# Kernel tuning notes

Hardware: AMD Instinct MI355X
Metric: run time of the kernel (lower is better)

The kernel has to match this reference:

```python
import jax, jax.numpy as jnp
import numpy as np


def _params_to_tokens(params):
    # (batch, 2k) -> (batch, k, 2) : chunk into freqs/amps then stack
    freqs, amps = jnp.split(params, 2, axis=-1)
    return jnp.stack((freqs, amps), axis=-1)


def setup_inputs() -> dict:
    key = jax.random.key(0)
    k1, k2 = jax.random.split(key)
    predicted = jax.random.normal(k1, (64, 4096), dtype=jnp.float32)
    target = jax.random.normal(k2, (64, 4096), dtype=jnp.float32)
    return {"predicted": predicted, "target": target}


def reference(predicted, target):
    p = _params_to_tokens(predicted)   # (b, k, 2)
    t = _params_to_tokens(target)      # (b, k, 2)
    # Euclidean cdist via gram-matrix identity (avoids (b,k,k,2) broadcast temp)
    p2 = jnp.sum(p * p, axis=-1)       # (b, k)
    t2 = jnp.sum(t * t, axis=-1)       # (b, k)
    gram = jnp.einsum('bid,bjd->bij', p, t)  # (b, k, k)
    sq = p2[:, :, None] + t2[:, None, :] - 2.0 * gram
    costs = jnp.sqrt(jnp.maximum(sq, 0.0))   # (b, k, k)
    min1 = jnp.mean(jnp.min(costs, axis=1), axis=-1)  # min over predicted dim
    min2 = jnp.mean(jnp.min(costs, axis=2), axis=-1)  # min over target dim
    return jnp.mean(min1 + min2)
```

## Files before the change

kernel.cpp:

```cpp
#include <hip/hip_runtime.h>


typedef _Float16 f16;
typedef _Float16 f16x8 __attribute__((ext_vector_type(8)));
typedef float f32x16 __attribute__((ext_vector_type(16)));

constexpr int K = 2048;
constexpr int BLOCK = 512;
constexpr int NBAND = 8;
constexpr int BAND = 256;
constexpr int NJT = K / 32;
constexpr unsigned INF_U = 0x7F800000u;

#define MFMA16 __builtin_amdgcn_mfma_f32_32x32x16_f16

__device__ __forceinline__ unsigned pk(f16 lo, f16 hi) {
  unsigned a = (unsigned)__builtin_bit_cast(unsigned short, lo);
  unsigned b = (unsigned)__builtin_bit_cast(unsigned short, hi);
  return a | (b << 16);
}
__device__ __forceinline__ unsigned split2(float v) {
  const f16 h = (f16)v;
  const f16 l = (f16)(v - (float)h);
  return pk(h, l);
}
__device__ __forceinline__ unsigned duplo(unsigned u) { return (u & 0xffffu) | (u << 16); }
__device__ __forceinline__ unsigned duphi(unsigned u) { return (u >> 16) | (u & 0xffff0000u); }
__device__ __forceinline__ f16x8 bcast4(unsigned d) {
  uint4 t = make_uint4(d, d, d, d);
  return __builtin_bit_cast(f16x8, t);
}
__device__ __forceinline__ float min3p(float a, float b, float c) {
  return fminf(fminf(a, b), c);
}

__global__ __launch_bounds__(BLOCK, 4) void chamfer_mfma(
    const float* __restrict__ pred, const float* __restrict__ targ,
    float* __restrict__ out, float* __restrict__ ws) {
  const int iband = blockIdx.x;
  const int b = blockIdx.y;
  const int tid = threadIdx.x;
  const int lane = tid & 63;
  const int w = tid >> 6;
  const int r = lane & 31;

  __shared__ uint4 Brec[K];
  __shared__ uint4 Arec[BAND];
  __shared__ unsigned colmin_u[K];
  __shared__ float wsum[8];

  const float* tb = targ + (size_t)b * (2 * K);
  const float* pb = pred + (size_t)b * (2 * K);

  #pragma unroll
  for (int k = 0; k < K / BLOCK; ++k) {
    const int j = tid + k * BLOCK;
    const float x = tb[j], y = tb[K + j];
    Brec[j] = make_uint4(split2(x), split2(y), split2(fmaf(x, x, y * y)), 0u);
    colmin_u[j] = INF_U;
  }
  if (tid < BAND) {
    const int i = iband * BAND + tid;
    const float x = pb[i], y = pb[K + i];
    Arec[tid] = make_uint4(split2(-2.0f * x), split2(-2.0f * y),
                           split2(fmaf(x, x, y * y)), 0u);
  }
  __syncthreads();

  const f32x16 zero = {};
  const unsigned umask = (lane < 32) ? 0xFFFFFFFFu : 0u;
  const unsigned umask_lo = umask & 0xFFFFu;

  const uint4 ra = Arec[w * 32 + r];
  const f16x8 aUH = bcast4(duplo(ra.x)), aUL = bcast4(duphi(ra.x));
  const f16x8 aWH = bcast4(duplo(ra.y)), aWL = bcast4(duphi(ra.y));
  const f16x8 aONE = bcast4(0x3C003C00u);

  uint4 bs = make_uint4(0x3C00u & umask, 0u, 0u, 0u);
  f32x16 seed = MFMA16(bcast4(duplo(ra.z)), __builtin_bit_cast(f16x8, bs),
                       zero, 0, 0, 0);
  seed = MFMA16(bcast4(duphi(ra.z)), __builtin_bit_cast(f16x8, bs),
                seed, 0, 0, 0);

  f32x16 rowacc;
  #pragma unroll
  for (int q = 0; q < 16; ++q) rowacc[q] = 3.4e38f;

  uint4 bq0 = make_uint4(0u, 0u, 0u, 0u);
  uint4 bq1 = make_uint4(0u, 0u, 0u, 0u);

  for (int jt = 0; jt < NJT; jt += 2) {
    const uint4 rb0 = Brec[jt * 32 + r];
    const uint4 rb1 = Brec[jt * 32 + 32 + r];

    bq0.x = rb0.x & umask;
    f32x16 d0 = MFMA16(aUH, __builtin_bit_cast(f16x8, bq0), seed, 0, 0, 0);
    bq0.x = rb0.x & umask_lo;
    d0 = MFMA16(aUL, __builtin_bit_cast(f16x8, bq0), d0, 0, 0, 0);
    bq0.x = rb0.y & umask;
    d0 = MFMA16(aWH, __builtin_bit_cast(f16x8, bq0), d0, 0, 0, 0);
    bq0.x = rb0.y & umask_lo;
    d0 = MFMA16(aWL, __builtin_bit_cast(f16x8, bq0), d0, 0, 0, 0);
    bq0.x = rb0.z & umask;
    d0 = MFMA16(aONE, __builtin_bit_cast(f16x8, bq0), d0, 0, 0, 0);

    bq1.x = rb1.x & umask;
    f32x16 d1 = MFMA16(aUH, __builtin_bit_cast(f16x8, bq1), seed, 0, 0, 0);
    bq1.x = rb1.x & umask_lo;
    d1 = MFMA16(aUL, __builtin_bit_cast(f16x8, bq1), d1, 0, 0, 0);
    bq1.x = rb1.y & umask;
    d1 = MFMA16(aWH, __builtin_bit_cast(f16x8, bq1), d1, 0, 0, 0);
    bq1.x = rb1.y & umask_lo;
    d1 = MFMA16(aWL, __builtin_bit_cast(f16x8, bq1), d1, 0, 0, 0);
    bq1.x = rb1.z & umask;
    d1 = MFMA16(aONE, __builtin_bit_cast(f16x8, bq1), d1, 0, 0, 0);

    #pragma unroll
    for (int q = 0; q < 16; ++q)
      rowacc[q] = min3p(rowacc[q], d0[q], d1[q]);

    {
      const float a0 = min3p(d0[0], d0[1], d0[2]);
      const float a1 = min3p(d0[3], d0[4], d0[5]);
      const float a2 = min3p(d0[6], d0[7], d0[8]);
      const float a3 = min3p(d0[9], d0[10], d0[11]);
      const float a4 = min3p(d0[12], d0[13], d0[14]);
      float cm = fminf(min3p(a0, a1, a2), min3p(a3, a4, d0[15]));
      cm = fminf(cm, __shfl_xor(cm, 32, 64));
      cm = fmaxf(cm, 0.0f);
      if (lane < 32) atomicMin(&colmin_u[jt * 32 + r], __float_as_uint(cm));
    }
    {
      const float a0 = min3p(d1[0], d1[1], d1[2]);
      const float a1 = min3p(d1[3], d1[4], d1[5]);
      const float a2 = min3p(d1[6], d1[7], d1[8]);
      const float a3 = min3p(d1[9], d1[10], d1[11]);
      const float a4 = min3p(d1[12], d1[13], d1[14]);
      float cm = fminf(min3p(a0, a1, a2), min3p(a3, a4, d1[15]));
      cm = fminf(cm, __shfl_xor(cm, 32, 64));
      cm = fmaxf(cm, 0.0f);
      if (lane < 32) atomicMin(&colmin_u[jt * 32 + 32 + r], __float_as_uint(cm));
    }
  }

  #pragma unroll
  for (int m = 1; m <= 16; m <<= 1) {
    #pragma unroll
    for (int q = 0; q < 16; ++q)
      rowacc[q] = fminf(rowacc[q], __shfl_xor(rowacc[q], m, 64));
  }
  float s = 0.0f;
  #pragma unroll
  for (int q = 0; q < 16; ++q) s += sqrtf(fmaxf(rowacc[q], 0.0f));
  s += __shfl_xor(s, 32, 64);
  if (lane == 0) wsum[w] = s;
  __syncthreads();
  if (tid == 0) {
    float t = 0.0f;
    #pragma unroll
    for (int i = 0; i < 8; ++i) t += wsum[i];
    atomicAdd(out, t * (1.0f / 131072.0f));
  }
  float* wrow = ws + (size_t)(b * NBAND + iband) * K;
  #pragma unroll
  for (int k = 0; k < K / BLOCK; ++k) {
    const int j = tid + k * BLOCK;
    wrow[j] = __uint_as_float(colmin_u[j]);
  }
}

__global__ __launch_bounds__(256, 4) void chamfer_pass2(
    const float* __restrict__ ws, float* __restrict__ out) {
  const int b = blockIdx.x;
  const int tid = threadIdx.x;
  __shared__ float wsum[4];
  const float* wrow = ws + (size_t)b * NBAND * K;
  float s = 0.0f;
  #pragma unroll
  for (int k = 0; k < K / 256; ++k) {
    const int j = tid + k * 256;
    float m = wrow[j];
    #pragma unroll
    for (int band = 1; band < NBAND; ++band) m = fminf(m, wrow[band * K + j]);
    s += sqrtf(m);
  }
  #pragma unroll
  for (int off = 32; off; off >>= 1) s += __shfl_down(s, off, 64);
  const int lane = tid & 63, w = tid >> 6;
  if (lane == 0) wsum[w] = s;
  __syncthreads();
  if (tid == 0)
    atomicAdd(out, (wsum[0] + wsum[1] + wsum[2] + wsum[3]) * (1.0f / 131072.0f));
}

extern "C" void kernel_launch(void* const* d_in, const int* in_sizes, int n_in,
                              void* d_out, int out_size, void* d_ws, size_t ws_size,
                              hipStream_t stream) {
  const float* pred = (const float*)d_in[0];
  const float* targ = (const float*)d_in[1];
  float* out = (float*)d_out;
  float* ws = (float*)d_ws;

  dim3 g1(NBAND, 64);
  chamfer_mfma<<<g1, dim3(BLOCK), 0, stream>>>(pred, targ, out, ws);
  chamfer_pass2<<<dim3(64), dim3(256), 0, stream>>>(ws, out);
}
```

Before: 93.80 us.

## Pack all distance terms into one MFMA K-dimension per tile

Replaces the five chained MFMAs per 32x32 tile (one per split term) and the seed MFMAs with a single 32x32x16 MFMA. The hi/lo fp16 split products, the squared norms and the ones column are packed across the 16-element K dimension using both lane halves. This cuts matrix-instruction count and the accumulator dependency chain about fivefold. The cost is extra per-iteration integer packing and lane selects, and the change relies on the packed operand layout exactly matching the MFMA K-index mapping.

```diff
diff --git a/kernel.cpp b/kernel.cpp
--- a/kernel.cpp
+++ b/kernel.cpp
@@ -24,12 +24,6 @@
   const f16 l = (f16)(v - (float)h);
   return pk(h, l);
 }
-__device__ __forceinline__ unsigned duplo(unsigned u) { return (u & 0xffffu) | (u << 16); }
-__device__ __forceinline__ unsigned duphi(unsigned u) { return (u >> 16) | (u & 0xffff0000u); }
-__device__ __forceinline__ f16x8 bcast4(unsigned d) {
-  uint4 t = make_uint4(d, d, d, d);
-  return __builtin_bit_cast(f16x8, t);
-}
 __device__ __forceinline__ float min3p(float a, float b, float c) {
   return fminf(fminf(a, b), c);
 }
@@ -43,6 +37,7 @@
   const int lane = tid & 63;
   const int w = tid >> 6;
   const int r = lane & 31;
+  const bool lo_half = (lane < 32);
 
   __shared__ uint4 Brec[K];
   __shared__ uint4 Arec[BAND];
@@ -68,52 +63,37 @@
   __syncthreads();
 
   const f32x16 zero = {};
-  const unsigned umask = (lane < 32) ? 0xFFFFFFFFu : 0u;
-  const unsigned umask_lo = umask & 0xFFFFu;
 
   const uint4 ra = Arec[w * 32 + r];
-  const f16x8 aUH = bcast4(duplo(ra.x)), aUL = bcast4(duphi(ra.x));
-  const f16x8 aWH = bcast4(duplo(ra.y)), aWL = bcast4(duphi(ra.y));
-  const f16x8 aONE = bcast4(0x3C003C00u);
-
-  uint4 bs = make_uint4(0x3C00u & umask, 0u, 0u, 0u);
-  f32x16 seed = MFMA16(bcast4(duplo(ra.z)), __builtin_bit_cast(f16x8, bs),
-                       zero, 0, 0, 0);
-  seed = MFMA16(bcast4(duphi(ra.z)), __builtin_bit_cast(f16x8, bs),
-                seed, 0, 0, 0);
+  const uint4 alo = make_uint4((ra.x & 0xffffu) | (ra.x << 16),
+                               (ra.x >> 16) | (ra.y << 16),
+                               ra.y,
+                               0x3C003C00u);
+  const uint4 ahi = make_uint4(ra.z, 0u, 0u, 0u);
+  const f16x8 af = __builtin_bit_cast(f16x8, lo_half ? alo : ahi);
+  const uint4 bhiq = make_uint4(0x3C003C00u, 0u, 0u, 0u);
 
   f32x16 rowacc;
   #pragma unroll
   for (int q = 0; q < 16; ++q) rowacc[q] = 3.4e38f;
 
-  uint4 bq0 = make_uint4(0u, 0u, 0u, 0u);
-  uint4 bq1 = make_uint4(0u, 0u, 0u, 0u);
-
   for (int jt = 0; jt < NJT; jt += 2) {
     const uint4 rb0 = Brec[jt * 32 + r];
     const uint4 rb1 = Brec[jt * 32 + 32 + r];
 
-    bq0.x = rb0.x & umask;
-    f32x16 d0 = MFMA16(aUH, __builtin_bit_cast(f16x8, bq0), seed, 0, 0, 0);
-    bq0.x = rb0.x & umask_lo;
-    d0 = MFMA16(aUL, __builtin_bit_cast(f16x8, bq0), d0, 0, 0, 0);
-    bq0.x = rb0.y & umask;
-    d0 = MFMA16(aWH, __builtin_bit_cast(f16x8, bq0), d0, 0, 0, 0);
-    bq0.x = rb0.y & umask_lo;
-    d0 = MFMA16(aWL, __builtin_bit_cast(f16x8, bq0), d0, 0, 0, 0);
-    bq0.x = rb0.z & umask;
-    d0 = MFMA16(aONE, __builtin_bit_cast(f16x8, bq0), d0, 0, 0, 0);
+    const uint4 b0 = make_uint4(rb0.x,
+                                (rb0.x & 0xffffu) | (rb0.y << 16),
+                                (rb0.y >> 16) | (rb0.y << 16),
+                                rb0.z);
+    const uint4 b1 = make_uint4(rb1.x,
+                                (rb1.x & 0xffffu) | (rb1.y << 16),
+                                (rb1.y >> 16) | (rb1.y << 16),
+                                rb1.z);
+    const f16x8 bf0 = __builtin_bit_cast(f16x8, lo_half ? b0 : bhiq);
+    const f16x8 bf1 = __builtin_bit_cast(f16x8, lo_half ? b1 : bhiq);
 
-    bq1.x = rb1.x & umask;
-    f32x16 d1 = MFMA16(aUH, __builtin_bit_cast(f16x8, bq1), seed, 0, 0, 0);
-    bq1.x = rb1.x & umask_lo;
-    d1 = MFMA16(aUL, __builtin_bit_cast(f16x8, bq1), d1, 0, 0, 0);
-    bq1.x = rb1.y & umask;
-    d1 = MFMA16(aWH, __builtin_bit_cast(f16x8, bq1), d1, 0, 0, 0);
-    bq1.x = rb1.y & umask_lo;
-    d1 = MFMA16(aWL, __builtin_bit_cast(f16x8, bq1), d1, 0, 0, 0);
-    bq1.x = rb1.z & umask;
-    d1 = MFMA16(aONE, __builtin_bit_cast(f16x8, bq1), d1, 0, 0, 0);
+    const f32x16 d0 = MFMA16(af, bf0, zero, 0, 0, 0);
+    const f32x16 d1 = MFMA16(af, bf1, zero, 0, 0, 0);
 
     #pragma unroll
     for (int q = 0; q < 16; ++q)
```

Result: faster. 85.23 us (-9.1%).
